# Kernel tuning notes

Hardware: AMD Instinct MI355X
Metric: run time of the kernel (lower is better)

The kernel has to match this reference:

```python
import jax, jax.numpy as jnp
import numpy as np

N_NODES = 100000
N_EDGES = 600000
D = 128
BN_EPS = 1e-5


def setup_inputs() -> dict:
    key = jax.random.key(0)
    k1, k2, k3 = jax.random.split(key, 3)
    x = jax.random.normal(k1, (N_NODES, D), dtype=jnp.float32)
    edge_index = jax.random.randint(k2, (2, N_EDGES), 0, N_NODES, dtype=jnp.int64)
    # Linear(in=D, out=D): kaiming-uniform-ish init
    W = jax.random.normal(k3, (D, D), dtype=jnp.float32) / np.sqrt(D)
    b = jnp.zeros((D,), dtype=jnp.float32)
    eps_gin = jnp.zeros((), dtype=jnp.float32)  # train_eps=True, init 0
    gamma = jnp.ones((D,), dtype=jnp.float32)
    beta = jnp.zeros((D,), dtype=jnp.float32)
    return {"x": x, "edge_index": edge_index, "W": W, "b": b,
            "eps_gin": eps_gin, "gamma": gamma, "beta": beta}


def reference(x, edge_index, W, b, eps_gin, gamma, beta):
    src, dst = edge_index[0], edge_index[1]
    # GIN aggregation: sum of source features into destination nodes
    agg = jax.ops.segment_sum(x[src], dst, num_segments=N_NODES)  # [N, D]
    h = (1.0 + eps_gin) * x + agg
    # MLP([D, D]) == single Linear (PyG plain_last)
    h = jnp.einsum('nd,df->nf', h, W.T) + b  # torch Linear: h @ W^T + b
    # BatchNorm1d in training mode (batch stats, biased variance)
    mean = jnp.mean(h, axis=0)
    var = jnp.mean((h - mean) ** 2, axis=0)
    h = (h - mean) * jax.lax.rsqrt(var + BN_EPS) * gamma + beta
    h = jax.nn.relu(h)
    # residual
    return h + x
```

## Files before the change

### kernel.cpp

```cpp
#include <hip/hip_runtime.h>
#include <hip/hip_bf16.h>

#define N_NODES 100000
#define N_EDGES 600000
#define D 128
#define BN_EPS 1e-5f
#define CAP 32
#define GEMM_BLOCKS 1024
#define GEMM_NSLOTS (GEMM_BLOCKS * 2)
#define FILL_THREADS 150000
#define ZS_BLOCKS 256

typedef __bf16 bf16x8 __attribute__((ext_vector_type(8)));
typedef float floatx4 __attribute__((ext_vector_type(4)));
typedef unsigned short ushortx8 __attribute__((ext_vector_type(8)));

__device__ __forceinline__ unsigned short f2bf(float f) {
    union { float f; unsigned u; } v; v.f = f;
    unsigned u = v.u;
    unsigned r = u + 0x7FFFu + ((u >> 16) & 1u);
    return (unsigned short)(r >> 16);
}
__device__ __forceinline__ float bflo(unsigned u) {
    union { unsigned u; float f; } v; v.u = u << 16; return v.f;
}
__device__ __forceinline__ float bfhi(unsigned u) {
    union { unsigned u; float f; } v; v.u = u & 0xFFFF0000u; return v.f;
}

__global__ __launch_bounds__(256) void k_fill(const int* __restrict__ ei,
                                              int* __restrict__ cursor,
                                              int* __restrict__ bucket) {
    int base = blockIdx.x * 256 + threadIdx.x;
    if (base >= FILL_THREADS) return;
    int e0 = base, e1 = base + FILL_THREADS, e2 = base + 2 * FILL_THREADS,
        e3 = base + 3 * FILL_THREADS;
    int s0 = ei[e0], s1 = ei[e1], s2 = ei[e2], s3 = ei[e3];
    int d0 = ei[N_EDGES + e0], d1 = ei[N_EDGES + e1],
        d2 = ei[N_EDGES + e2], d3 = ei[N_EDGES + e3];
    int p0 = atomicAdd(&cursor[d0], 1);
    int p1 = atomicAdd(&cursor[d1], 1);
    int p2 = atomicAdd(&cursor[d2], 1);
    int p3 = atomicAdd(&cursor[d3], 1);
    if (p0 < CAP) bucket[d0 * CAP + p0] = s0;
    if (p1 < CAP) bucket[d1 * CAP + p1] = s1;
    if (p2 < CAP) bucket[d2 * CAP + p2] = s2;
    if (p3 < CAP) bucket[d3 * CAP + p3] = s3;
}

__global__ __launch_bounds__(256) void k_gemm_y(const float* __restrict__ x,
                                                const float* __restrict__ W,
                                                unsigned short* __restrict__ y) {
    const int lane = threadIdx.x & 63;
    const int wid  = threadIdx.x >> 6;
    const int gw   = blockIdx.x * 4 + wid;
    const int fhalf = gw & 1;
    const int pair  = gw >> 1;
    const int n16  = lane & 15;
    const int quad = lane >> 4;
    const int fbase = fhalf * 64;

    bf16x8 B[4][4];
#pragma unroll
    for (int ft = 0; ft < 4; ++ft) {
#pragma unroll
        for (int ks = 0; ks < 4; ++ks) {
            const float* wp = W + (fbase + ft * 16 + n16) * D + ks * 32 + quad * 8;
            float4 wa = *(const float4*)wp;
            float4 wb = *(const float4*)(wp + 4);
            ushortx8 u;
            u[0] = f2bf(wa.x); u[1] = f2bf(wa.y); u[2] = f2bf(wa.z); u[3] = f2bf(wa.w);
            u[4] = f2bf(wb.x); u[5] = f2bf(wb.y); u[6] = f2bf(wb.z); u[7] = f2bf(wb.w);
            B[ft][ks] = __builtin_bit_cast(bf16x8, u);
        }
    }

    for (int chunk = pair; chunk < N_NODES / 16; chunk += GEMM_NSLOTS) {
        const int rbase = chunk * 16;
        floatx4 acc[4];
#pragma unroll
        for (int ft = 0; ft < 4; ++ft) acc[ft] = (floatx4){0.f, 0.f, 0.f, 0.f};

#pragma unroll
        for (int ks = 0; ks < 4; ++ks) {
            const float* xp = x + (size_t)(rbase + n16) * D + ks * 32 + quad * 8;
            float4 xa = *(const float4*)xp;
            float4 xb4 = *(const float4*)(xp + 4);
            ushortx8 u;
            u[0] = f2bf(xa.x); u[1] = f2bf(xa.y); u[2] = f2bf(xa.z); u[3] = f2bf(xa.w);
            u[4] = f2bf(xb4.x); u[5] = f2bf(xb4.y); u[6] = f2bf(xb4.z); u[7] = f2bf(xb4.w);
            bf16x8 a = __builtin_bit_cast(bf16x8, u);
#pragma unroll
            for (int ft = 0; ft < 4; ++ft)
                acc[ft] = __builtin_amdgcn_mfma_f32_16x16x32_bf16(a, B[ft][ks], acc[ft], 0, 0, 0);
        }

#pragma unroll
        for (int ft = 0; ft < 4; ++ft) {
            const int col = fbase + ft * 16 + n16;
#pragma unroll
            for (int i = 0; i < 4; ++i)
                y[(size_t)(rbase + quad * 4 + i) * D + col] = f2bf(acc[ft][i]);
        }
    }
}

__global__ __launch_bounds__(256) void k_agg(const int* __restrict__ cursor,
                                             const int* __restrict__ bucket,
                                             const unsigned short* __restrict__ y,
                                             const float* __restrict__ epsp,
                                             unsigned short* __restrict__ zb) {
    int tid = blockIdx.x * 256 + threadIdx.x;
    int node = tid >> 5;
    if (node >= N_NODES) return;
    int lane = tid & 31;
    int deg = cursor[node];
    if (deg > CAP) deg = CAP;
    const int* bk = bucket + node * CAP;

    float4 a0 = make_float4(0.f, 0.f, 0.f, 0.f);
    float4 a1 = a0, a2 = a0, a3 = a0, a4 = a0, a5 = a0, a6 = a0, a7 = a0;

    for (int i = 0; i < deg; i += 8) {
        int rem = deg - i, last = rem - 1;
        int s0 = bk[i];
        int s1 = bk[i + (1 < rem ? 1 : last)];
        int s2 = bk[i + (2 < rem ? 2 : last)];
        int s3 = bk[i + (3 < rem ? 3 : last)];
        int s4 = bk[i + (4 < rem ? 4 : last)];
        int s5 = bk[i + (5 < rem ? 5 : last)];
        int s6 = bk[i + (6 < rem ? 6 : last)];
        int s7 = bk[i + (7 < rem ? 7 : last)];
        uint2 v0 = ((const uint2*)(y + (size_t)s0 * D))[lane];
        uint2 v1 = ((const uint2*)(y + (size_t)s1 * D))[lane];
        uint2 v2 = ((const uint2*)(y + (size_t)s2 * D))[lane];
        uint2 v3 = ((const uint2*)(y + (size_t)s3 * D))[lane];
        uint2 v4 = ((const uint2*)(y + (size_t)s4 * D))[lane];
        uint2 v5 = ((const uint2*)(y + (size_t)s5 * D))[lane];
        uint2 v6 = ((const uint2*)(y + (size_t)s6 * D))[lane];
        uint2 v7 = ((const uint2*)(y + (size_t)s7 * D))[lane];
        a0.x += bflo(v0.x); a0.y += bfhi(v0.x); a0.z += bflo(v0.y); a0.w += bfhi(v0.y);
        if (1 < rem) { a1.x += bflo(v1.x); a1.y += bfhi(v1.x); a1.z += bflo(v1.y); a1.w += bfhi(v1.y); }
        if (2 < rem) { a2.x += bflo(v2.x); a2.y += bfhi(v2.x); a2.z += bflo(v2.y); a2.w += bfhi(v2.y); }
        if (3 < rem) { a3.x += bflo(v3.x); a3.y += bfhi(v3.x); a3.z += bflo(v3.y); a3.w += bfhi(v3.y); }
        if (4 < rem) { a4.x += bflo(v4.x); a4.y += bfhi(v4.x); a4.z += bflo(v4.y); a4.w += bfhi(v4.y); }
        if (5 < rem) { a5.x += bflo(v5.x); a5.y += bfhi(v5.x); a5.z += bflo(v5.y); a5.w += bfhi(v5.y); }
        if (6 < rem) { a6.x += bflo(v6.x); a6.y += bfhi(v6.x); a6.z += bflo(v6.y); a6.w += bfhi(v6.y); }
        if (7 < rem) { a7.x += bflo(v7.x); a7.y += bfhi(v7.x); a7.z += bflo(v7.y); a7.w += bfhi(v7.y); }
    }
    float r0 = ((a0.x + a1.x) + (a2.x + a3.x)) + ((a4.x + a5.x) + (a6.x + a7.x));
    float r1 = ((a0.y + a1.y) + (a2.y + a3.y)) + ((a4.y + a5.y) + (a6.y + a7.y));
    float r2 = ((a0.z + a1.z) + (a2.z + a3.z)) + ((a4.z + a5.z) + (a6.z + a7.z));
    float r3 = ((a0.w + a1.w) + (a2.w + a3.w)) + ((a4.w + a5.w) + (a6.w + a7.w));

    const float one_eps = 1.0f + epsp[0];
    uint2 yv = ((const uint2*)(y + (size_t)node * D))[lane];
    ushort4 o;
    o.x = f2bf(one_eps * bflo(yv.x) + r0);
    o.y = f2bf(one_eps * bfhi(yv.x) + r1);
    o.z = f2bf(one_eps * bflo(yv.y) + r2);
    o.w = f2bf(one_eps * bfhi(yv.y) + r3);
    ((ushort4*)(zb + (size_t)node * D))[lane] = o;
}

__global__ __launch_bounds__(256) void k_zstats(const unsigned short* __restrict__ zb,
                                                float* __restrict__ pscr) {
    const int t = threadIdx.x;
    const int lane = t & 31;
    const int slot = t >> 5;

    float psum[4] = {0.f, 0.f, 0.f, 0.f};
    float psq[4]  = {0.f, 0.f, 0.f, 0.f};

    for (int node = blockIdx.x * 8 + slot; node < N_NODES; node += ZS_BLOCKS * 8) {
        uint2 zv = ((const uint2*)(zb + (size_t)node * D))[lane];
        float z0 = bflo(zv.x), z1 = bfhi(zv.x), z2 = bflo(zv.y), z3 = bfhi(zv.y);
        psum[0] += z0; psq[0] += z0 * z0;
        psum[1] += z1; psq[1] += z1 * z1;
        psum[2] += z2; psq[2] += z2 * z2;
        psum[3] += z3; psq[3] += z3 * z3;
    }

    __shared__ float sred[8][32][9];
#pragma unroll
    for (int j = 0; j < 4; ++j) {
        sred[slot][lane][j]     = psum[j];
        sred[slot][lane][4 + j] = psq[j];
    }
    __syncthreads();
    {
        const int c = t & 127;
        const int j = (t < 128) ? (c & 3) : 4 + (c & 3);
        const int l = c >> 2;
        float acc = 0.f;
#pragma unroll
        for (int s = 0; s < 8; ++s)
            acc += sred[s][l][j];
        pscr[(size_t)blockIdx.x * 256 + t] = acc;
    }
}

__global__ __launch_bounds__(256) void k_scsh(const float* __restrict__ pscr,
                                              const float* __restrict__ gamma,
                                              const float* __restrict__ beta,
                                              float* __restrict__ scsh) {
    const int t = threadIdx.x;
    float acc = 0.f;
    for (int r = 0; r < ZS_BLOCKS; ++r)
        acc += pscr[(size_t)r * 256 + t];
    __shared__ float red[256];
    red[t] = acc;
    __syncthreads();
    if (t < 128) {
        const float inv_n = 1.0f / (float)N_NODES;
        float mean = red[t] * inv_n;
        float var  = red[128 + t] * inv_n - mean * mean;
        float s    = gamma[t] * rsqrtf(var + BN_EPS);
        scsh[t]       = s;
        scsh[128 + t] = beta[t] - mean * s;
    }
}

__global__ __launch_bounds__(256) void k_final(const unsigned short* __restrict__ zb,
                                               const float* __restrict__ x,
                                               const float* __restrict__ scsh,
                                               float* __restrict__ out) {
    __shared__ float scs[128], shs[128];
    const int t = threadIdx.x;
    if (t < 128) scs[t] = scsh[t];
    else         shs[t - 128] = scsh[t];
    __syncthreads();

    for (size_t i = (size_t)blockIdx.x * 256 + t; i < (size_t)N_NODES * D / 4;
         i += (size_t)gridDim.x * 256) {
        const size_t idx = i * 4;
        const int f = (int)(idx & (D - 1));
        uint2 zv = *(const uint2*)(zb + idx);
        float4 xv = *(const float4*)(x + idx);
        float z0 = bflo(zv.x), z1 = bfhi(zv.x), z2 = bflo(zv.y), z3 = bfhi(zv.y);
        float4 o;
        o.x = fmaxf(z0 * scs[f]     + shs[f],     0.f) + xv.x;
        o.y = fmaxf(z1 * scs[f + 1] + shs[f + 1], 0.f) + xv.y;
        o.z = fmaxf(z2 * scs[f + 2] + shs[f + 2], 0.f) + xv.z;
        o.w = fmaxf(z3 * scs[f + 3] + shs[f + 3], 0.f) + xv.w;
        *(float4*)(out + idx) = o;
    }
}

extern "C" void kernel_launch(void* const* d_in, const int* in_sizes, int n_in,
                              void* d_out, int out_size, void* d_ws, size_t ws_size,
                              hipStream_t stream) {
    const float* x     = (const float*)d_in[0];
    const int*   ei    = (const int*)d_in[1];
    const float* W     = (const float*)d_in[2];
    const float* epsp  = (const float*)d_in[4];
    const float* gamma = (const float*)d_in[5];
    const float* beta  = (const float*)d_in[6];
    float* out = (float*)d_out;

    char* ws = (char*)d_ws;
    int*   cursor = (int*)ws;
    int*   bucket = (int*)(ws + 400128ull);
    unsigned short* y  = (unsigned short*)(ws + 13200128ull);
    unsigned short* zb = (unsigned short*)(ws + 38800128ull);
    float* scsh = (float*)(ws + 64400128ull);
    float* pscr = (float*)bucket;

    hipMemsetAsync(cursor, 0, 400000ull, stream);

    k_fill<<<(FILL_THREADS + 255) / 256, 256, 0, stream>>>(ei, cursor, bucket);
    k_gemm_y<<<GEMM_BLOCKS, 256, 0, stream>>>(x, W, y);
    k_agg<<<(N_NODES * 32 + 255) / 256, 256, 0, stream>>>(cursor, bucket, y, epsp, zb);
    k_zstats<<<ZS_BLOCKS, 256, 0, stream>>>(zb, pscr);
    k_scsh<<<1, 256, 0, stream>>>(pscr, gamma, beta, scsh);
    k_final<<<2048, 256, 0, stream>>>(zb, x, scsh, out);
}
```

Before: 244.2 us.

## Merge edge bucketing and GEMM into one launch, prefetch next x chunk

The edge-bucketing fill kernel and the bf16 MFMA GEMM kernel become one launch, with block index choosing the role, so the atomic-heavy fill can run alongside the bandwidth-bound GEMM and one launch boundary goes away. Inside the GEMM loop, the x rows for the next chunk are loaded before the current chunk's MFMAs, a software double-buffer meant to hide global load latency. This costs more registers for the prefetch buffers, which may lower occupancy, and the GEMM grid-stride slots stay unchanged.

```diff
diff --git a/kernel.cpp b/kernel.cpp
--- a/kernel.cpp
+++ b/kernel.cpp
@@ -8,7 +8,9 @@
 #define CAP 32
 #define GEMM_BLOCKS 1024
 #define GEMM_NSLOTS (GEMM_BLOCKS * 2)
+#define NCHUNK (N_NODES / 16)
 #define FILL_THREADS 150000
+#define FILL_BLOCKS ((FILL_THREADS + 255) / 256)
 #define ZS_BLOCKS 256
 
 typedef __bf16 bf16x8 __attribute__((ext_vector_type(8)));
@@ -28,32 +30,41 @@
     union { unsigned u; float f; } v; v.u = u & 0xFFFF0000u; return v.f;
 }
 
-__global__ __launch_bounds__(256) void k_fill(const int* __restrict__ ei,
-                                              int* __restrict__ cursor,
-                                              int* __restrict__ bucket) {
-    int base = blockIdx.x * 256 + threadIdx.x;
-    if (base >= FILL_THREADS) return;
-    int e0 = base, e1 = base + FILL_THREADS, e2 = base + 2 * FILL_THREADS,
-        e3 = base + 3 * FILL_THREADS;
-    int s0 = ei[e0], s1 = ei[e1], s2 = ei[e2], s3 = ei[e3];
-    int d0 = ei[N_EDGES + e0], d1 = ei[N_EDGES + e1],
-        d2 = ei[N_EDGES + e2], d3 = ei[N_EDGES + e3];
-    int p0 = atomicAdd(&cursor[d0], 1);
-    int p1 = atomicAdd(&cursor[d1], 1);
-    int p2 = atomicAdd(&cursor[d2], 1);
-    int p3 = atomicAdd(&cursor[d3], 1);
-    if (p0 < CAP) bucket[d0 * CAP + p0] = s0;
-    if (p1 < CAP) bucket[d1 * CAP + p1] = s1;
-    if (p2 < CAP) bucket[d2 * CAP + p2] = s2;
-    if (p3 < CAP) bucket[d3 * CAP + p3] = s3;
-}
-
-__global__ __launch_bounds__(256) void k_gemm_y(const float* __restrict__ x,
-                                                const float* __restrict__ W,
-                                                unsigned short* __restrict__ y) {
+#define CONV8(dst, fa, fb) { ushortx8 _u;                                   \
+    _u[0] = f2bf((fa).x); _u[1] = f2bf((fa).y);                             \
+    _u[2] = f2bf((fa).z); _u[3] = f2bf((fa).w);                             \
+    _u[4] = f2bf((fb).x); _u[5] = f2bf((fb).y);                             \
+    _u[6] = f2bf((fb).z); _u[7] = f2bf((fb).w);                             \
+    dst = __builtin_bit_cast(bf16x8, _u); }
+
+__global__ __launch_bounds__(256) void k_fill_gemm(const int* __restrict__ ei,
+                                                   int* __restrict__ cursor,
+                                                   int* __restrict__ bucket,
+                                                   const float* __restrict__ x,
+                                                   const float* __restrict__ W,
+                                                   unsigned short* __restrict__ y) {
+    if (blockIdx.x < FILL_BLOCKS) {
+        int base = blockIdx.x * 256 + threadIdx.x;
+        if (base >= FILL_THREADS) return;
+        int e0 = base, e1 = base + FILL_THREADS, e2 = base + 2 * FILL_THREADS,
+            e3 = base + 3 * FILL_THREADS;
+        int s0 = ei[e0], s1 = ei[e1], s2 = ei[e2], s3 = ei[e3];
+        int d0 = ei[N_EDGES + e0], d1 = ei[N_EDGES + e1],
+            d2 = ei[N_EDGES + e2], d3 = ei[N_EDGES + e3];
+        int p0 = atomicAdd(&cursor[d0], 1);
+        int p1 = atomicAdd(&cursor[d1], 1);
+        int p2 = atomicAdd(&cursor[d2], 1);
+        int p3 = atomicAdd(&cursor[d3], 1);
+        if (p0 < CAP) bucket[d0 * CAP + p0] = s0;
+        if (p1 < CAP) bucket[d1 * CAP + p1] = s1;
+        if (p2 < CAP) bucket[d2 * CAP + p2] = s2;
+        if (p3 < CAP) bucket[d3 * CAP + p3] = s3;
+        return;
+    }
+
     const int lane = threadIdx.x & 63;
     const int wid  = threadIdx.x >> 6;
-    const int gw   = blockIdx.x * 4 + wid;
+    const int gw   = (blockIdx.x - FILL_BLOCKS) * 4 + wid;
     const int fhalf = gw & 1;
     const int pair  = gw >> 1;
     const int n16  = lane & 15;
@@ -68,33 +79,56 @@
             const float* wp = W + (fbase + ft * 16 + n16) * D + ks * 32 + quad * 8;
             float4 wa = *(const float4*)wp;
             float4 wb = *(const float4*)(wp + 4);
-            ushortx8 u;
-            u[0] = f2bf(wa.x); u[1] = f2bf(wa.y); u[2] = f2bf(wa.z); u[3] = f2bf(wa.w);
-            u[4] = f2bf(wb.x); u[5] = f2bf(wb.y); u[6] = f2bf(wb.z); u[7] = f2bf(wb.w);
-            B[ft][ks] = __builtin_bit_cast(bf16x8, u);
+            bf16x8 bb; CONV8(bb, wa, wb);
+            B[ft][ks] = bb;
         }
     }
 
-    for (int chunk = pair; chunk < N_NODES / 16; chunk += GEMM_NSLOTS) {
+    int chunk = pair;
+    float4 ca0, ca1, ca2, ca3, cb0, cb1, cb2, cb3;
+    {
+        const float* xp = x + (size_t)(chunk * 16 + n16) * D + quad * 8;
+        ca0 = *(const float4*)(xp);       cb0 = *(const float4*)(xp + 4);
+        ca1 = *(const float4*)(xp + 32);  cb1 = *(const float4*)(xp + 36);
+        ca2 = *(const float4*)(xp + 64);  cb2 = *(const float4*)(xp + 68);
+        ca3 = *(const float4*)(xp + 96);  cb3 = *(const float4*)(xp + 100);
+    }
+    while (true) {
+        const int nchunk = chunk + GEMM_NSLOTS;
+        const bool hn = nchunk < NCHUNK;
+        float4 na0, na1, na2, na3, nb0, nb1, nb2, nb3;
+        if (hn) {
+            const float* xp = x + (size_t)(nchunk * 16 + n16) * D + quad * 8;
+            na0 = *(const float4*)(xp);       nb0 = *(const float4*)(xp + 4);
+            na1 = *(const float4*)(xp + 32);  nb1 = *(const float4*)(xp + 36);
+            na2 = *(const float4*)(xp + 64);  nb2 = *(const float4*)(xp + 68);
+            na3 = *(const float4*)(xp + 96);  nb3 = *(const float4*)(xp + 100);
+        }
+
+        floatx4 acc[4];
+#pragma unroll
+        for (int ft = 0; ft < 4; ++ft) acc[ft] = (floatx4){0.f, 0.f, 0.f, 0.f};
+        {
+            bf16x8 a;
+            CONV8(a, ca0, cb0);
+#pragma unroll
+            for (int ft = 0; ft < 4; ++ft)
+                acc[ft] = __builtin_amdgcn_mfma_f32_16x16x32_bf16(a, B[ft][0], acc[ft], 0, 0, 0);
+            CONV8(a, ca1, cb1);
+#pragma unroll
+            for (int ft = 0; ft < 4; ++ft)
+                acc[ft] = __builtin_amdgcn_mfma_f32_16x16x32_bf16(a, B[ft][1], acc[ft], 0, 0, 0);
+            CONV8(a, ca2, cb2);
+#pragma unroll
+            for (int ft = 0; ft < 4; ++ft)
+                acc[ft] = __builtin_amdgcn_mfma_f32_16x16x32_bf16(a, B[ft][2], acc[ft], 0, 0, 0);
+            CONV8(a, ca3, cb3);
+#pragma unroll
+            for (int ft = 0; ft < 4; ++ft)
+                acc[ft] = __builtin_amdgcn_mfma_f32_16x16x32_bf16(a, B[ft][3], acc[ft], 0, 0, 0);
+        }
+
         const int rbase = chunk * 16;
-        floatx4 acc[4];
-#pragma unroll
-        for (int ft = 0; ft < 4; ++ft) acc[ft] = (floatx4){0.f, 0.f, 0.f, 0.f};
-
-#pragma unroll
-        for (int ks = 0; ks < 4; ++ks) {
-            const float* xp = x + (size_t)(rbase + n16) * D + ks * 32 + quad * 8;
-            float4 xa = *(const float4*)xp;
-            float4 xb4 = *(const float4*)(xp + 4);
-            ushortx8 u;
-            u[0] = f2bf(xa.x); u[1] = f2bf(xa.y); u[2] = f2bf(xa.z); u[3] = f2bf(xa.w);
-            u[4] = f2bf(xb4.x); u[5] = f2bf(xb4.y); u[6] = f2bf(xb4.z); u[7] = f2bf(xb4.w);
-            bf16x8 a = __builtin_bit_cast(bf16x8, u);
-#pragma unroll
-            for (int ft = 0; ft < 4; ++ft)
-                acc[ft] = __builtin_amdgcn_mfma_f32_16x16x32_bf16(a, B[ft][ks], acc[ft], 0, 0, 0);
-        }
-
 #pragma unroll
         for (int ft = 0; ft < 4; ++ft) {
             const int col = fbase + ft * 16 + n16;
@@ -102,6 +136,11 @@
             for (int i = 0; i < 4; ++i)
                 y[(size_t)(rbase + quad * 4 + i) * D + col] = f2bf(acc[ft][i]);
         }
+
+        if (!hn) break;
+        ca0 = na0; ca1 = na1; ca2 = na2; ca3 = na3;
+        cb0 = nb0; cb1 = nb1; cb2 = nb2; cb3 = nb3;
+        chunk = nchunk;
     }
 }
 
@@ -268,8 +307,7 @@
 
     hipMemsetAsync(cursor, 0, 400000ull, stream);
 
-    k_fill<<<(FILL_THREADS + 255) / 256, 256, 0, stream>>>(ei, cursor, bucket);
-    k_gemm_y<<<GEMM_BLOCKS, 256, 0, stream>>>(x, W, y);
+    k_fill_gemm<<<FILL_BLOCKS + GEMM_BLOCKS, 256, 0, stream>>>(ei, cursor, bucket, x, W, y);
     k_agg<<<(N_NODES * 32 + 255) / 256, 256, 0, stream>>>(cursor, bucket, y, epsp, zb);
     k_zstats<<<ZS_BLOCKS, 256, 0, stream>>>(zb, pscr);
     k_scsh<<<1, 256, 0, stream>>>(pscr, gamma, beta, scsh);
```

Result: faster. 237.6 us (-2.7%).
